# Kernel optimization log

Hardware: AMD Instinct MI355X
Metric: run time of the kernel (lower is better)

## Reference

```python
import jax, jax.numpy as jnp
import numpy as np

TOP_K = 2
CAPACITY_FACTOR = 1.0


def _ffn(x, w1, w2):
    # SwiGLU FFN: x [N, D], w1 [D, 2F], w2 [F, D]
    h = x @ w1
    x1, x2 = jnp.split(h, 2, axis=-1)
    return (x1 * jax.nn.silu(x2)) @ w2


def setup_inputs() -> dict:
    key = jax.random.key(0)
    ks = jax.random.split(key, 6)
    B, S, D, F, E_r, E_s = 4, 2048, 2048, 1024, 7, 1
    sc_in = 1.0 / np.sqrt(D)
    sc_mid = 1.0 / np.sqrt(F)
    return {
        "x": jax.random.normal(ks[0], (B, S, D), dtype=jnp.float32),
        "gate_w": jax.random.normal(ks[1], (D, E_r), dtype=jnp.float32) * sc_in,
        "expert_bias": jnp.zeros((E_r,), dtype=jnp.float32),
        "shared_w1": jax.random.normal(ks[2], (E_s, D, 2 * F), dtype=jnp.float32) * sc_in,
        "shared_w2": jax.random.normal(ks[3], (E_s, F, D), dtype=jnp.float32) * sc_mid,
        "routed_w1": jax.random.normal(ks[4], (E_r, D, 2 * F), dtype=jnp.float32) * sc_in,
        "routed_w2": jax.random.normal(ks[5], (E_r, F, D), dtype=jnp.float32) * sc_mid,
    }


def reference(x, gate_w, expert_bias, shared_w1, shared_w2, routed_w1, routed_w2):
    B, S, D = x.shape
    E_r = gate_w.shape[1]
    T = B * S
    capacity = max(1, int(CAPACITY_FACTOR * T / E_r))
    flat_x = x.reshape(T, D)

    # shared experts: applied to every token, summed
    shared_sum = jax.vmap(_ffn, in_axes=(None, 0, 0))(flat_x, shared_w1, shared_w2).sum(0)

    # gating (eval mode: no noise, no dropout)
    gate_logits = flat_x @ gate_w + expert_bias  # [T, E_r]
    aff = jax.nn.sigmoid(gate_logits)
    _, topk_idx = jax.lax.top_k(aff, TOP_K)  # [T, K]
    # mask[t, e] = expert e is among token t's top-k
    mask = (topk_idx[:, :, None] == jnp.arange(E_r)[None, None, :]).any(axis=1)  # [T, E_r]

    # per-expert capacity selection: keep top-`capacity` masked tokens by affinity
    score = jnp.where(mask, aff, -1.0).T  # [E_r, T]; aff >= 0 so -1 sorts last
    _, sel_idx = jax.lax.top_k(score, capacity)  # [E_r, capacity] token ids
    kept = jnp.take_along_axis(mask.T, sel_idx, axis=1)  # [E_r, cap]
    w = jnp.where(kept, jnp.take_along_axis(aff.T, sel_idx, axis=1), 0.0)  # [E_r, cap]

    # grouped gather -> FFN -> weighted scatter-add
    inp = flat_x[sel_idx]  # [E_r, cap, D]
    out = jax.vmap(_ffn)(inp, routed_w1, routed_w2)  # [E_r, cap, D]
    routed_sum = jnp.zeros_like(flat_x).at[sel_idx].add(out * w[:, :, None])

    return (shared_sum + routed_sum).reshape(B, S, D)
```

## Files before the change

kernel.cpp:

```cpp
#include <hip/hip_runtime.h>
#include <hip/hip_bf16.h>

typedef unsigned long long u64;
typedef __bf16 bf16x8 __attribute__((ext_vector_type(8)));
typedef float f32x4 __attribute__((ext_vector_type(4)));
typedef unsigned short ushort8_t __attribute__((ext_vector_type(8)));

#define TOKS 8192
#define DMODEL 2048
#define FD 1024
#define NEXP 7
#define CAP 1170
#define CAPP 1280
#define URT 134

#define MFMA16(a, b, c) __builtin_amdgcn_mfma_f32_16x16x32_bf16(a, b, c, 0, 0, 0)

__device__ __forceinline__ unsigned short f2bf(float f) {
  __hip_bfloat16 b = __float2bfloat16(f);
  return __builtin_bit_cast(unsigned short, b);
}
__device__ __forceinline__ float bf2f(unsigned short u) {
  __hip_bfloat16 b = __builtin_bit_cast(__hip_bfloat16, u);
  return __bfloat162float(b);
}
__device__ __forceinline__ void gload_lds16(const void* g, void* l) {
  __builtin_amdgcn_global_load_lds(
      (const __attribute__((address_space(1))) void*)g,
      (__attribute__((address_space(3))) void*)l, 16, 0, 0);
}

__global__ __launch_bounds__(256) void k_conv_gate(
    const float* __restrict__ x, const float* __restrict__ gw,
    const float* __restrict__ bias, unsigned short* __restrict__ xb,
    u64* __restrict__ keys) {
  const int t = blockIdx.x;
  const int tid = threadIdx.x;
  const int lane = tid & 63, wv = tid >> 6;
  const float* xr = x + (long)t * DMODEL;
  const int i0 = tid * 8;
  float4 v0 = *(const float4*)&xr[i0];
  float4 v1 = *(const float4*)&xr[i0 + 4];
  float xv[8] = {v0.x, v0.y, v0.z, v0.w, v1.x, v1.y, v1.z, v1.w};
  ushort8_t o;
#pragma unroll
  for (int j = 0; j < 8; ++j) o[j] = f2bf(xv[j]);
  *(ushort8_t*)&xb[(long)t * DMODEL + i0] = o;
  double acc[NEXP];
#pragma unroll
  for (int e = 0; e < NEXP; ++e) acc[e] = 0.0;
#pragma unroll
  for (int j = 0; j < 8; ++j) {
    const float* g = gw + (long)(i0 + j) * NEXP;
    double xd = (double)xv[j];
#pragma unroll
    for (int e = 0; e < NEXP; ++e) acc[e] += xd * (double)g[e];
  }
#pragma unroll
  for (int e = 0; e < NEXP; ++e)
    for (int off = 32; off > 0; off >>= 1)
      acc[e] += __shfl_down(acc[e], off, 64);
  __shared__ double red[4][NEXP];
  if (lane == 0)
#pragma unroll
    for (int e = 0; e < NEXP; ++e) red[wv][e] = acc[e];
  __syncthreads();
  if (tid == 0) {
    float aff[NEXP];
#pragma unroll
    for (int e = 0; e < NEXP; ++e) {
      double lg = red[0][e] + red[1][e] + red[2][e] + red[3][e] + (double)bias[e];
      aff[e] = (float)(1.0 / (1.0 + exp(-lg)));
    }
    int i1 = 0;
    for (int e = 1; e < NEXP; ++e) if (aff[e] > aff[i1]) i1 = e;
    int i2 = -1;
    for (int e = 0; e < NEXP; ++e) {
      if (e == i1) continue;
      if (i2 < 0 || aff[e] > aff[i2]) i2 = e;
    }
#pragma unroll
    for (int e = 0; e < NEXP; ++e) {
      u64 key = (u64)(0xFFFFFFFFu - (unsigned)t);
      if (e == i1 || e == i2) key |= ((u64)__float_as_uint(aff[e])) << 32;
      keys[(long)e * TOKS + t] = key;
    }
  }
}

template <bool PERM>
__global__ void k_transpose_bf16(const float* __restrict__ in0,
                                 const float* __restrict__ inr,
                                 unsigned short* __restrict__ out,
                                 int R, int C) {
  __shared__ float tile[32][33];
  int z = blockIdx.z;
  const float* in = (z == 0) ? in0 : (inr + (long)(z - 1) * R * C);
  unsigned short* o = out + (long)z * R * C;
  int c0 = blockIdx.x * 32;
  int r0 = blockIdx.y * 32;
  int tx = threadIdx.x, ty = threadIdx.y;
#pragma unroll
  for (int k = 0; k < 4; ++k)
    tile[ty + 8 * k][tx] = in[(long)(r0 + ty + 8 * k) * C + c0 + tx];
  __syncthreads();
#pragma unroll
  for (int k = 0; k < 4; ++k) {
    int c = c0 + ty + 8 * k;
    long orow = PERM ? (long)(((c & 1023) >> 4) * 32 + ((c >> 10) << 4) + (c & 15))
                     : (long)c;
    o[orow * R + r0 + tx] = f2bf(tile[tx][ty + 8 * k]);
  }
}

__global__ __launch_bounds__(1024) void k_select(
    const u64* __restrict__ keys, int* __restrict__ sel,
    float* __restrict__ selw, unsigned* __restrict__ cnt,
    int* __restrict__ inv) {
  __shared__ unsigned hist[256];
  __shared__ u64 s_prefix;
  __shared__ unsigned s_k;
  __shared__ unsigned s_cnt;
  const int e = blockIdx.x;
  const u64* kk = keys + (long)e * TOKS;
  const int tid = threadIdx.x;
  if (tid == 0) { s_prefix = 0; s_k = CAP; s_cnt = 0; }
  __syncthreads();
  for (int shift = 56; shift >= 0; shift -= 8) {
    if (tid < 256) hist[tid] = 0;
    __syncthreads();
    u64 pref = s_prefix;
    for (int i = tid; i < TOKS; i += 1024) {
      u64 key = kk[i];
      bool match = (shift == 56) || ((key >> (shift + 8)) == pref);
      if (match) atomicAdd(&hist[(unsigned)(key >> shift) & 255u], 1u);
    }
    __syncthreads();
    if (tid == 0) {
      unsigned k = s_k, cum = 0;
      for (int b = 255; b >= 0; --b) {
        unsigned c = hist[b];
        if (cum + c >= k) {
          s_prefix = (s_prefix << 8) | (unsigned)b;
          s_k = k - cum;
          break;
        }
        cum += c;
      }
    }
    __syncthreads();
  }
  const u64 T = s_prefix;
  for (int i = tid; i < TOKS; i += 1024) {
    u64 key = kk[i];
    if (key >= T) {
      unsigned p = atomicAdd(&s_cnt, 1u);
      int tok = (int)(0xFFFFFFFFu - (unsigned)(key & 0xFFFFFFFFull));
      unsigned vb = (unsigned)(key >> 32);
      sel[e * CAPP + p] = tok;
      selw[e * CAPP + p] = vb ? __uint_as_float(vb) : 0.0f;
      if (vb) {
        unsigned pos = atomicAdd(&cnt[tok], 1u);
        inv[tok * 2 + pos] = e * CAPP + (int)p;
      }
    }
  }
  for (int i = CAP + tid; i < CAPP; i += 1024) {
    sel[e * CAPP + i] = 0;
    selw[e * CAPP + i] = 0.0f;
  }
}

__global__ __launch_bounds__(256) void k_combine(
    float* __restrict__ out, const unsigned short* __restrict__ rout,
    const int* __restrict__ inv, const unsigned* __restrict__ cnt) {
  const int tok = blockIdx.x;
  const unsigned c = cnt[tok];
  if (c == 0) return;
  int i0 = inv[tok * 2];
  int i1 = (c > 1) ? inv[tok * 2 + 1] : -1;
  if (c > 1 && i1 < i0) { int t = i0; i0 = i1; i1 = t; }
  const int col = threadIdx.x * 8;
  float* o = out + (long)tok * DMODEL + col;
  float4 v0 = *(float4*)o;
  float4 v1 = *(float4*)(o + 4);
  ushort8_t r0 = *(const ushort8_t*)&rout[(long)i0 * DMODEL + col];
  v0.x += bf2f(r0[0]); v0.y += bf2f(r0[1]); v0.z += bf2f(r0[2]); v0.w += bf2f(r0[3]);
  v1.x += bf2f(r0[4]); v1.y += bf2f(r0[5]); v1.z += bf2f(r0[6]); v1.w += bf2f(r0[7]);
  if (c > 1) {
    ushort8_t r1 = *(const ushort8_t*)&rout[(long)i1 * DMODEL + col];
    v0.x += bf2f(r1[0]); v0.y += bf2f(r1[1]); v0.z += bf2f(r1[2]); v0.w += bf2f(r1[3]);
    v1.x += bf2f(r1[4]); v1.y += bf2f(r1[5]); v1.z += bf2f(r1[6]); v1.w += bf2f(r1[7]);
  }
  *(float4*)o = v0;
  *(float4*)(o + 4) = v1;
}

template <int WHICH>
__global__ __launch_bounds__(256, 4) void k_ffn(
    const unsigned short* __restrict__ Abase,
    const unsigned short* __restrict__ Wbase,
    unsigned short* __restrict__ a_all, float* __restrict__ out,
    unsigned short* __restrict__ r_out,
    const int* __restrict__ sel, const float* __restrict__ selw) {
  constexpr int K = (WHICH == 1) ? DMODEL : FD;
  constexpr int N = (WHICH == 1) ? 2 * FD : DMODEL;
  constexpr int nk = K >> 5;
  __shared__ unsigned short lds[2][8192];
  const int tid = threadIdx.x;
  const int w = tid >> 6;
  const int lane = tid & 63;

  int lin = blockIdx.x + ((int)blockIdx.y << 4);
  int gt = (lin & 7) * 268 + (lin >> 3);
  int ct, rt;
  int su;
  if (gt < 2048) { su = gt >> 7; int rr = gt & 127; ct = rr >> 3; rt = rr & 7; }
  else           { su = 16;      int rr = gt - 2048; ct = rr / 6; rt = rr % 6; }
  const int by_u = su * 8 + rt;
  const int bx = ct;

  int e, zw, m0l;
  if (by_u < 64) { e = -1; zw = 0; m0l = by_u << 7; }
  else { int q = by_u - 64; e = q / 10; zw = e + 1; m0l = (q % 10) << 7; }
  const long crow0_u = (e < 0) ? (long)m0l : (8192 + (long)e * CAPP + m0l);
  const long n0 = (long)bx * 128;
  const unsigned short* Bm = Wbase + (long)zw * N * K;

  const int r_ = (w << 4) + (lane >> 2);
  const int p_ = lane & 3;
  const unsigned short* aSrc[2];
  const unsigned short* bSrc[2];
#pragma unroll
  for (int c = 0; c < 2; ++c) {
    int rsg = c * 64 + r_;
    int q = p_ ^ ((rsg >> 1) & 3);
    long arow;
    if (WHICH == 1)
      arow = (e < 0) ? (long)(m0l + rsg) : (long)sel[e * CAPP + m0l + rsg];
    else
      arow = crow0_u + rsg;
    aSrc[c] = Abase + arow * (long)K + q * 8;
    bSrc[c] = Bm + (n0 + rsg) * (long)K + q * 8;
  }
  const int dst0 = tid * 8;

  auto STAGE = [&](int buf, int kt) {
    const long ko = (long)kt * 32;
#pragma unroll
    for (int c = 0; c < 2; ++c) {
      gload_lds16(aSrc[c] + ko, &lds[buf][c * 2048 + dst0]);
      gload_lds16(bSrc[c] + ko, &lds[buf][4096 + c * 2048 + dst0]);
    }
  };

  const int wr = w >> 1, wc = w & 1;
  const int lr = lane & 15, kq = lane >> 4;
  const int slot = (kq ^ ((lr >> 1) & 3)) * 8;
  const int aRow = wr * 64 + lr;
  const int bRow = wc * 64 + lr;

  STAGE(0, 0);
  asm volatile("s_waitcnt vmcnt(0)" ::: "memory");
  __builtin_amdgcn_sched_barrier(0);
  __builtin_amdgcn_s_barrier();
  __builtin_amdgcn_sched_barrier(0);

  f32x4 acc[4][4] = {};
  int cur = 0;

#pragma unroll 1
  for (int kt = 0; kt < nk; ++kt) {
    if (kt + 1 < nk) STAGE(cur ^ 1, kt + 1);
    const unsigned short* aSeg = &lds[cur][0];
    const unsigned short* bSeg = &lds[cur][4096];
    bf16x8 af[4], bf[4];
#pragma unroll
    for (int m = 0; m < 4; ++m)
      af[m] = *(const bf16x8*)&aSeg[(aRow + m * 16) * 32 + slot];
#pragma unroll
    for (int n = 0; n < 4; ++n)
      bf[n] = *(const bf16x8*)&bSeg[(bRow + n * 16) * 32 + slot];
    asm volatile("s_waitcnt lgkmcnt(0)" ::: "memory");
    __builtin_amdgcn_sched_barrier(0);
    __builtin_amdgcn_s_setprio(1);
#pragma unroll
    for (int m = 0; m < 4; ++m)
#pragma unroll
      for (int n = 0; n < 4; ++n)
        acc[m][n] = MFMA16(af[m], bf[n], acc[m][n]);
    __builtin_amdgcn_s_setprio(0);
    asm volatile("s_waitcnt vmcnt(0)" ::: "memory");
    __builtin_amdgcn_sched_barrier(0);
    __builtin_amdgcn_s_barrier();
    __builtin_amdgcn_sched_barrier(0);
    cur ^= 1;
  }

  const int r0q = (lane >> 4) * 4;
  const int cc = lane & 15;

  if (WHICH == 1) {
    const long gcol0 = (n0 >> 1) + wc * 32;
#pragma unroll
    for (int m = 0; m < 4; ++m)
#pragma unroll
      for (int rj = 0; rj < 4; ++rj) {
        long row = crow0_u + wr * 64 + m * 16 + r0q + rj;
#pragma unroll
        for (int q2 = 0; q2 < 2; ++q2) {
          float x1v = acc[m][2 * q2][rj];
          float x2v = acc[m][2 * q2 + 1][rj];
          float s = x2v / (1.0f + __expf(-x2v));
          a_all[row * FD + gcol0 + q2 * 16 + cc] = f2bf(x1v * s);
        }
      }
  } else {
    const long ccol0 = n0 + wc * 64;
    if (e < 0) {
#pragma unroll
      for (int m = 0; m < 4; ++m)
#pragma unroll
        for (int rj = 0; rj < 4; ++rj) {
          long row = m0l + wr * 64 + m * 16 + r0q + rj;
#pragma unroll
          for (int n = 0; n < 4; ++n)
            out[row * DMODEL + ccol0 + n * 16 + cc] = acc[m][n][rj];
        }
    } else {
#pragma unroll
      for (int m = 0; m < 4; ++m)
#pragma unroll
        for (int rj = 0; rj < 4; ++rj) {
          int lrow = m0l + wr * 64 + m * 16 + r0q + rj;
          float wgt = selw[e * CAPP + lrow];
          unsigned short* C = r_out + ((long)e * CAPP + lrow) * DMODEL;
#pragma unroll
          for (int n = 0; n < 4; ++n)
            C[ccol0 + n * 16 + cc] = f2bf(acc[m][n][rj] * wgt);
        }
    }
  }
}

extern "C" void kernel_launch(void* const* d_in, const int* in_sizes, int n_in,
                              void* d_out, int out_size, void* d_ws,
                              size_t ws_size, hipStream_t stream) {
  (void)in_sizes; (void)n_in; (void)out_size; (void)ws_size;
  const float* x = (const float*)d_in[0];
  const float* gw = (const float*)d_in[1];
  const float* eb = (const float*)d_in[2];
  const float* sw1 = (const float*)d_in[3];
  const float* sw2 = (const float*)d_in[4];
  const float* rw1 = (const float*)d_in[5];
  const float* rw2 = (const float*)d_in[6];
  float* out = (float*)d_out;

  char* ws = (char*)d_ws;
  size_t off = 0;
  auto alloc = [&](size_t bytes) {
    size_t o = off;
    off += (bytes + 255) & ~(size_t)255;
    return o;
  };
  unsigned short* xb    = (unsigned short*)(ws + alloc((size_t)TOKS * DMODEL * 2));
  unsigned short* w1t   = (unsigned short*)(ws + alloc((size_t)8 * DMODEL * (2 * FD) * 2));
  unsigned short* w2t   = (unsigned short*)(ws + alloc((size_t)8 * DMODEL * FD * 2));
  unsigned short* a_all = (unsigned short*)(ws + alloc((size_t)(TOKS + NEXP * CAPP) * FD * 2));
  unsigned short* r_out = (unsigned short*)(ws + alloc((size_t)NEXP * CAPP * DMODEL * 2));
  u64* keys = (u64*)(ws + alloc((size_t)NEXP * TOKS * 8));
  int* sel  = (int*)(ws + alloc((size_t)NEXP * CAPP * 4));
  float* selw = (float*)(ws + alloc((size_t)NEXP * CAPP * 4));
  unsigned* cnt = (unsigned*)(ws + alloc((size_t)TOKS * 4));
  int* inv = (int*)(ws + alloc((size_t)TOKS * 2 * 4));

  k_conv_gate<<<TOKS, 256, 0, stream>>>(x, gw, eb, xb, keys);
  dim3 tb(32, 8);
  k_transpose_bf16<true><<<dim3(64, 64, 8), tb, 0, stream>>>(sw1, rw1, w1t, DMODEL, 2 * FD);
  k_transpose_bf16<false><<<dim3(64, 32, 8), tb, 0, stream>>>(sw2, rw2, w2t, FD, DMODEL);
  hipMemsetAsync(cnt, 0, (size_t)TOKS * 4, stream);
  k_select<<<NEXP, 1024, 0, stream>>>(keys, sel, selw, cnt, inv);
  k_ffn<1><<<dim3(16, URT), 256, 0, stream>>>(xb, w1t, a_all, nullptr, nullptr,
                                              sel, nullptr);
  k_ffn<2><<<dim3(16, URT), 256, 0, stream>>>(a_all, w2t, nullptr, out, r_out,
                                              nullptr, selw);
  k_combine<<<TOKS, 256, 0, stream>>>(out, r_out, inv, cnt);
}
```

Before: 495.8 us.

## Enlarge FFN GEMM tiles to 256x128 with 512 threads and vectorize weight transpose

The FFN GEMM kernels move from 128x128 tiles with 256 threads to 256x128 tiles with 512 threads (8 waves), so each B tile is reused across twice as many rows. The block-to-tile mapping is rewritten so that each XCD gets a column pair. The weight transpose kernel switches to 64x64 tiles with float4 loads and 8-wide bf16 stores. The point is to cut global traffic for weights and speed up the conversion, at the cost of more LDS per block, which may lower occupancy. The unseen epilogue has to match the new row layout and the wave indexing (wr = w>>1 now spans 4 row groups), and that is not visible here.

```diff
diff --git a/kernel.cpp b/kernel.cpp
--- a/kernel.cpp
+++ b/kernel.cpp
@@ -12,7 +12,7 @@
 #define NEXP 7
 #define CAP 1170
 #define CAPP 1280
-#define URT 134
+#define URT256 67
 
 #define MFMA16(a, b, c) __builtin_amdgcn_mfma_f32_16x16x32_bf16(a, b, c, 0, 0, 0)
 
@@ -89,27 +89,39 @@
 }
 
 template <bool PERM>
-__global__ void k_transpose_bf16(const float* __restrict__ in0,
-                                 const float* __restrict__ inr,
-                                 unsigned short* __restrict__ out,
-                                 int R, int C) {
-  __shared__ float tile[32][33];
+__global__ __launch_bounds__(256) void k_transpose64(
+    const float* __restrict__ in0, const float* __restrict__ inr,
+    unsigned short* __restrict__ out, int R, int C) {
+  __shared__ unsigned short t[64][68];
   int z = blockIdx.z;
   const float* in = (z == 0) ? in0 : (inr + (long)(z - 1) * R * C);
   unsigned short* o = out + (long)z * R * C;
-  int c0 = blockIdx.x * 32;
-  int r0 = blockIdx.y * 32;
-  int tx = threadIdx.x, ty = threadIdx.y;
-#pragma unroll
-  for (int k = 0; k < 4; ++k)
-    tile[ty + 8 * k][tx] = in[(long)(r0 + ty + 8 * k) * C + c0 + tx];
+  const int c0 = blockIdx.x * 64;
+  const int r0 = blockIdx.y * 64;
+  const int tid = threadIdx.x;
+  const int lrow = tid >> 4;
+  const int lc4 = (tid & 15) * 4;
+#pragma unroll
+  for (int i = 0; i < 4; ++i) {
+    int r = lrow + i * 16;
+    float4 v = *(const float4*)&in[(long)(r0 + r) * C + c0 + lc4];
+    t[r][lc4 + 0] = f2bf(v.x);
+    t[r][lc4 + 1] = f2bf(v.y);
+    t[r][lc4 + 2] = f2bf(v.z);
+    t[r][lc4 + 3] = f2bf(v.w);
+  }
   __syncthreads();
-#pragma unroll
-  for (int k = 0; k < 4; ++k) {
-    int c = c0 + ty + 8 * k;
-    long orow = PERM ? (long)(((c & 1023) >> 4) * 32 + ((c >> 10) << 4) + (c & 15))
-                     : (long)c;
-    o[orow * R + r0 + tx] = f2bf(tile[tx][ty + 8 * k]);
+  const int lc = tid >> 2;
+  const int c = c0 + lc;
+  const long orow = PERM ? (long)(((c & 1023) >> 4) * 32 + ((c >> 10) << 4) + (c & 15))
+                         : (long)c;
+#pragma unroll
+  for (int j = 0; j < 2; ++j) {
+    int rloc = ((tid & 3) + j * 4) * 8;
+    ushort8_t o8;
+#pragma unroll
+    for (int q = 0; q < 8; ++q) o8[q] = t[rloc + q][lc];
+    *(ushort8_t*)&o[orow * R + r0 + rloc] = o8;
   }
 }
 
@@ -197,7 +209,7 @@
 }
 
 template <int WHICH>
-__global__ __launch_bounds__(256, 4) void k_ffn(
+__global__ __launch_bounds__(512, 4) void k_ffn(
     const unsigned short* __restrict__ Abase,
     const unsigned short* __restrict__ Wbase,
     unsigned short* __restrict__ a_all, float* __restrict__ out,
@@ -206,52 +218,52 @@
   constexpr int K = (WHICH == 1) ? DMODEL : FD;
   constexpr int N = (WHICH == 1) ? 2 * FD : DMODEL;
   constexpr int nk = K >> 5;
-  __shared__ unsigned short lds[2][8192];
+  constexpr int ASH = 256 * 32;
+  __shared__ unsigned short lds[2][ASH + 128 * 32];
   const int tid = threadIdx.x;
   const int w = tid >> 6;
   const int lane = tid & 63;
 
   int lin = blockIdx.x + ((int)blockIdx.y << 4);
-  int gt = (lin & 7) * 268 + (lin >> 3);
-  int ct, rt;
-  int su;
-  if (gt < 2048) { su = gt >> 7; int rr = gt & 127; ct = rr >> 3; rt = rr & 7; }
-  else           { su = 16;      int rr = gt - 2048; ct = rr / 6; rt = rr % 6; }
-  const int by_u = su * 8 + rt;
-  const int bx = ct;
+  int xcd = lin & 7;
+  int tt = lin >> 3;
+  int colh = (tt >= URT256) ? 1 : 0;
+  int by_u = tt - colh * URT256;
+  int bx = xcd * 2 + colh;
 
   int e, zw, m0l;
-  if (by_u < 64) { e = -1; zw = 0; m0l = by_u << 7; }
-  else { int q = by_u - 64; e = q / 10; zw = e + 1; m0l = (q % 10) << 7; }
+  if (by_u < 32) { e = -1; zw = 0; m0l = by_u << 8; }
+  else { int q = by_u - 32; e = q / 5; zw = e + 1; m0l = (q % 5) << 8; }
   const long crow0_u = (e < 0) ? (long)m0l : (8192 + (long)e * CAPP + m0l);
   const long n0 = (long)bx * 128;
   const unsigned short* Bm = Wbase + (long)zw * N * K;
 
-  const int r_ = (w << 4) + (lane >> 2);
-  const int p_ = lane & 3;
   const unsigned short* aSrc[2];
-  const unsigned short* bSrc[2];
-#pragma unroll
-  for (int c = 0; c < 2; ++c) {
-    int rsg = c * 64 + r_;
-    int q = p_ ^ ((rsg >> 1) & 3);
+  const unsigned short* bSrc;
+#pragma unroll
+  for (int j = 0; j < 2; ++j) {
+    int r = w * 32 + j * 16 + (lane >> 2);
+    int q = (lane & 3) ^ ((r >> 1) & 3);
     long arow;
     if (WHICH == 1)
-      arow = (e < 0) ? (long)(m0l + rsg) : (long)sel[e * CAPP + m0l + rsg];
+      arow = (e < 0) ? (long)(m0l + r) : (long)sel[e * CAPP + m0l + r];
     else
-      arow = crow0_u + rsg;
-    aSrc[c] = Abase + arow * (long)K + q * 8;
-    bSrc[c] = Bm + (n0 + rsg) * (long)K + q * 8;
-  }
-  const int dst0 = tid * 8;
+      arow = crow0_u + r;
+    aSrc[j] = Abase + arow * (long)K + q * 8;
+  }
+  {
+    int r = w * 16 + (lane >> 2);
+    int q = (lane & 3) ^ ((r >> 1) & 3);
+    bSrc = Bm + (n0 + r) * (long)K + q * 8;
+  }
+  const int dstA0 = (w * 128 + lane) * 8;
+  const int dstB0 = ASH + (w * 64 + lane) * 8;
 
   auto STAGE = [&](int buf, int kt) {
     const long ko = (long)kt * 32;
-#pragma unroll
-    for (int c = 0; c < 2; ++c) {
-      gload_lds16(aSrc[c] + ko, &lds[buf][c * 2048 + dst0]);
-      gload_lds16(bSrc[c] + ko, &lds[buf][4096 + c * 2048 + dst0]);
-    }
+    gload_lds16(aSrc[0] + ko, &lds[buf][dstA0]);
+    gload_lds16(aSrc[1] + ko, &lds[buf][dstA0 + 512]);
+    gload_lds16(bSrc + ko, &lds[buf][dstB0]);
   };
 
   const int wr = w >> 1, wc = w & 1;
@@ -273,7 +285,7 @@
   for (int kt = 0; kt < nk; ++kt) {
     if (kt + 1 < nk) STAGE(cur ^ 1, kt + 1);
     const unsigned short* aSeg = &lds[cur][0];
-    const unsigned short* bSeg = &lds[cur][4096];
+    const unsigned short* bSeg = &lds[cur][ASH];
     bf16x8 af[4], bf[4];
 #pragma unroll
     for (int m = 0; m < 4; ++m)
@@ -375,14 +387,13 @@
   int* inv = (int*)(ws + alloc((size_t)TOKS * 2 * 4));
 
   k_conv_gate<<<TOKS, 256, 0, stream>>>(x, gw, eb, xb, keys);
-  dim3 tb(32, 8);
-  k_transpose_bf16<true><<<dim3(64, 64, 8), tb, 0, stream>>>(sw1, rw1, w1t, DMODEL, 2 * FD);
-  k_transpose_bf16<false><<<dim3(64, 32, 8), tb, 0, stream>>>(sw2, rw2, w2t, FD, DMODEL);
+  k_transpose64<true><<<dim3(32, 32, 8), 256, 0, stream>>>(sw1, rw1, w1t, DMODEL, 2 * FD);
+  k_transpose64<false><<<dim3(32, 16, 8), 256, 0, stream>>>(sw2, rw2, w2t, FD, DMODEL);
   hipMemsetAsync(cnt, 0, (size_t)TOKS * 4, stream);
   k_select<<<NEXP, 1024, 0, stream>>>(keys, sel, selw, cnt, inv);
-  k_ffn<1><<<dim3(16, URT), 256, 0, stream>>>(xb, w1t, a_all, nullptr, nullptr,
-                                              sel, nullptr);
-  k_ffn<2><<<dim3(16, URT), 256, 0, stream>>>(a_all, w2t, nullptr, out, r_out,
-                                              nullptr, selw);
+  k_ffn<1><<<dim3(16, URT256), 512, 0, stream>>>(xb, w1t, a_all, nullptr, nullptr,
+                                                 sel, nullptr);
+  k_ffn<2><<<dim3(16, URT256), 512, 0, stream>>>(a_all, w2t, nullptr, out, r_out,
+                                                 nullptr, selw);
   k_combine<<<TOKS, 256, 0, stream>>>(out, r_out, inv, cnt);
 }
```

New measurement: 521.0 us. 5.1% more time.

## Replace 128x128 FFN GEMM with 256x256 tile, 8-wave, interleaved LDS pipeline

Applied to the files above, without the earlier changes.

The two grouped FFN GEMM kernels move from 128x128 output tiles with 4 waves to 256x256 tiles with 8 waves (512 threads), a K-step of 64 and 128 KB of dynamic LDS. Loads are split into four segments (two A halves, two B halves) and issued between MFMA phases, so global-to-LDS transfers overlap compute within each iteration. The LDS layout uses an XOR swizzle. The larger tile raises arithmetic intensity and cuts redundant global traffic. In exchange the grid is much smaller, the old L2-friendly block remapping is dropped, and occupancy per CU is lower, which may hurt load balance and latency hiding. The 128 KB dynamic LDS launch also does not appear to raise any max-dynamic-shared-memory attribute.

```diff
diff --git a/kernel.cpp b/kernel.cpp
--- a/kernel.cpp
+++ b/kernel.cpp
@@ -12,7 +12,7 @@
 #define NEXP 7
 #define CAP 1170
 #define CAPP 1280
-#define URT 134
+#define URT256 67
 
 #define MFMA16(a, b, c) __builtin_amdgcn_mfma_f32_16x16x32_bf16(a, b, c, 0, 0, 0)
 
@@ -197,105 +197,175 @@
 }
 
 template <int WHICH>
-__global__ __launch_bounds__(256, 4) void k_ffn(
+__global__ __launch_bounds__(512, 2) void k_ffn8(
     const unsigned short* __restrict__ Abase,
     const unsigned short* __restrict__ Wbase,
     unsigned short* __restrict__ a_all, float* __restrict__ out,
     unsigned short* __restrict__ r_out,
     const int* __restrict__ sel, const float* __restrict__ selw) {
   constexpr int K = (WHICH == 1) ? DMODEL : FD;
-  constexpr int N = (WHICH == 1) ? 2 * FD : DMODEL;
-  constexpr int nk = K >> 5;
-  __shared__ unsigned short lds[2][8192];
+  constexpr int N = 2048;
+  constexpr int nk = K >> 6;
+  extern __shared__ unsigned short lds[];
   const int tid = threadIdx.x;
   const int w = tid >> 6;
   const int lane = tid & 63;
 
-  int lin = blockIdx.x + ((int)blockIdx.y << 4);
-  int gt = (lin & 7) * 268 + (lin >> 3);
-  int ct, rt;
-  int su;
-  if (gt < 2048) { su = gt >> 7; int rr = gt & 127; ct = rr >> 3; rt = rr & 7; }
-  else           { su = 16;      int rr = gt - 2048; ct = rr / 6; rt = rr % 6; }
-  const int by_u = su * 8 + rt;
-  const int bx = ct;
+  const int bx = blockIdx.x;
+  const int by_u = blockIdx.y;
 
   int e, zw, m0l;
-  if (by_u < 64) { e = -1; zw = 0; m0l = by_u << 7; }
-  else { int q = by_u - 64; e = q / 10; zw = e + 1; m0l = (q % 10) << 7; }
+  if (by_u < 32) { e = -1; zw = 0; m0l = by_u << 8; }
+  else { int q = by_u - 32; e = q / 5; zw = e + 1; m0l = (q % 5) << 8; }
   const long crow0_u = (e < 0) ? (long)m0l : (8192 + (long)e * CAPP + m0l);
-  const long n0 = (long)bx * 128;
+  const long n0 = (long)bx * 256;
   const unsigned short* Bm = Wbase + (long)zw * N * K;
 
-  const int r_ = (w << 4) + (lane >> 2);
-  const int p_ = lane & 3;
-  const unsigned short* aSrc[2];
-  const unsigned short* bSrc[2];
-#pragma unroll
-  for (int c = 0; c < 2; ++c) {
-    int rsg = c * 64 + r_;
-    int q = p_ ^ ((rsg >> 1) & 3);
-    long arow;
-    if (WHICH == 1)
-      arow = (e < 0) ? (long)(m0l + rsg) : (long)sel[e * CAPP + m0l + rsg];
-    else
-      arow = crow0_u + rsg;
-    aSrc[c] = Abase + arow * (long)K + q * 8;
-    bSrc[c] = Bm + (n0 + rsg) * (long)K + q * 8;
-  }
-  const int dst0 = tid * 8;
-
-  auto STAGE = [&](int buf, int kt) {
-    const long ko = (long)kt * 32;
-#pragma unroll
-    for (int c = 0; c < 2; ++c) {
-      gload_lds16(aSrc[c] + ko, &lds[buf][c * 2048 + dst0]);
-      gload_lds16(bSrc[c] + ko, &lds[buf][4096 + c * 2048 + dst0]);
-    }
+  const int wr = w >> 2;
+  const int wc = w & 3;
+  const int lr = lane & 15;
+  const int kq = lane >> 4;
+
+  const unsigned short* aP[2][2];
+  const unsigned short* bP[2][2];
+  int dstOff[2];
+#pragma unroll
+  for (int j = 0; j < 2; ++j) {
+    int L = w * 128 + j * 64 + lane;
+    int r = L >> 3;
+    int cEl = ((L & 7) * 8) ^ ((r & 7) * 8);
+    dstOff[j] = (w * 2 + j) * 512;
+#pragma unroll
+    for (int h = 0; h < 2; ++h) {
+      long ar;
+      if (WHICH == 1)
+        ar = (e < 0) ? (long)(m0l + h * 128 + r)
+                     : (long)sel[e * CAPP + m0l + h * 128 + r];
+      else
+        ar = crow0_u + h * 128 + r;
+      aP[h][j] = Abase + ar * (long)K + cEl;
+      bP[h][j] = Bm + (n0 + h * 128 + r) * (long)K + cEl;
+    }
+  }
+
+  auto STAGE = [&](int seg, int d, int ts) {
+    unsigned short* base = lds + ((d << 2) + seg) * 8192;
+    const unsigned short *p0, *p1;
+    if (seg < 2) { p0 = aP[seg][0]; p1 = aP[seg][1]; }
+    else         { p0 = bP[seg - 2][0]; p1 = bP[seg - 2][1]; }
+    long ko = (long)ts * 64;
+    gload_lds16(p0 + ko, base + dstOff[0]);
+    gload_lds16(p1 + ko, base + dstOff[1]);
   };
 
-  const int wr = w >> 1, wc = w & 1;
-  const int lr = lane & 15, kq = lane >> 4;
-  const int slot = (kq ^ ((lr >> 1) & 3)) * 8;
-  const int aRow = wr * 64 + lr;
-  const int bRow = wc * 64 + lr;
-
-  STAGE(0, 0);
-  asm volatile("s_waitcnt vmcnt(0)" ::: "memory");
+  const int aSegT = wr;
+  const int bSegT = 2 + (wc >> 1);
+  const int colSw0 = (kq * 8) ^ ((lr & 7) * 8);
+  const int colSw1 = (32 + kq * 8) ^ ((lr & 7) * 8);
+  const int bRow = (wc & 1) * 64 + lr;
+
+  STAGE(0, 0, 0); STAGE(1, 0, 0); STAGE(2, 0, 0); STAGE(3, 0, 0);
+  if (nk > 1) { STAGE(0, 1, 1); STAGE(1, 1, 1); }
+  else        { STAGE(0, 1, 0); STAGE(1, 1, 0); }
+  asm volatile("s_waitcnt vmcnt(4)" ::: "memory");
   __builtin_amdgcn_sched_barrier(0);
   __builtin_amdgcn_s_barrier();
   __builtin_amdgcn_sched_barrier(0);
 
-  f32x4 acc[4][4] = {};
-  int cur = 0;
+  f32x4 acc[8][4] = {};
 
 #pragma unroll 1
-  for (int kt = 0; kt < nk; ++kt) {
-    if (kt + 1 < nk) STAGE(cur ^ 1, kt + 1);
-    const unsigned short* aSeg = &lds[cur][0];
-    const unsigned short* bSeg = &lds[cur][4096];
-    bf16x8 af[4], bf[4];
-#pragma unroll
-    for (int m = 0; m < 4; ++m)
-      af[m] = *(const bf16x8*)&aSeg[(aRow + m * 16) * 32 + slot];
-#pragma unroll
-    for (int n = 0; n < 4; ++n)
-      bf[n] = *(const bf16x8*)&bSeg[(bRow + n * 16) * 32 + slot];
+  for (int T = 0; T < nk; ++T) {
+    const int d = T & 1, dn = d ^ 1;
+    int t1 = T + 1; if (t1 >= nk) t1 -= nk;
+    int t2 = T + 2; if (t2 >= nk) t2 -= nk;
+    const unsigned short* aSeg = lds + ((d << 2) + aSegT) * 8192;
+    const unsigned short* bSeg = lds + ((d << 2) + bSegT) * 8192;
+    bf16x8 af[8], b0, b1;
+
+#pragma unroll
+    for (int m = 0; m < 8; ++m)
+      af[m] = *(const bf16x8*)&aSeg[(m * 16 + lr) * 64 + colSw0];
+    b0 = *(const bf16x8*)&bSeg[(bRow + 0) * 64 + colSw0];
+    b1 = *(const bf16x8*)&bSeg[(bRow + 16) * 64 + colSw0];
+    __builtin_amdgcn_sched_barrier(0);
+    STAGE(2, dn, t1);
+    __builtin_amdgcn_sched_barrier(0);
+    __builtin_amdgcn_s_barrier();
     asm volatile("s_waitcnt lgkmcnt(0)" ::: "memory");
     __builtin_amdgcn_sched_barrier(0);
     __builtin_amdgcn_s_setprio(1);
 #pragma unroll
-    for (int m = 0; m < 4; ++m)
-#pragma unroll
-      for (int n = 0; n < 4; ++n)
-        acc[m][n] = MFMA16(af[m], bf[n], acc[m][n]);
+    for (int m = 0; m < 8; ++m) {
+      acc[m][0] = MFMA16(af[m], b0, acc[m][0]);
+      acc[m][1] = MFMA16(af[m], b1, acc[m][1]);
+    }
     __builtin_amdgcn_s_setprio(0);
-    asm volatile("s_waitcnt vmcnt(0)" ::: "memory");
-    __builtin_amdgcn_sched_barrier(0);
-    __builtin_amdgcn_s_barrier();
-    __builtin_amdgcn_sched_barrier(0);
-    cur ^= 1;
-  }
+    __builtin_amdgcn_sched_barrier(0);
+    __builtin_amdgcn_s_barrier();
+    __builtin_amdgcn_sched_barrier(0);
+
+    b0 = *(const bf16x8*)&bSeg[(bRow + 32) * 64 + colSw0];
+    b1 = *(const bf16x8*)&bSeg[(bRow + 48) * 64 + colSw0];
+    __builtin_amdgcn_sched_barrier(0);
+    STAGE(3, dn, t1);
+    __builtin_amdgcn_sched_barrier(0);
+    __builtin_amdgcn_s_barrier();
+    asm volatile("s_waitcnt lgkmcnt(0)" ::: "memory");
+    __builtin_amdgcn_sched_barrier(0);
+    __builtin_amdgcn_s_setprio(1);
+#pragma unroll
+    for (int m = 0; m < 8; ++m) {
+      acc[m][2] = MFMA16(af[m], b0, acc[m][2]);
+      acc[m][3] = MFMA16(af[m], b1, acc[m][3]);
+    }
+    __builtin_amdgcn_s_setprio(0);
+    __builtin_amdgcn_sched_barrier(0);
+    __builtin_amdgcn_s_barrier();
+    __builtin_amdgcn_sched_barrier(0);
+
+#pragma unroll
+    for (int m = 0; m < 8; ++m)
+      af[m] = *(const bf16x8*)&aSeg[(m * 16 + lr) * 64 + colSw1];
+    b0 = *(const bf16x8*)&bSeg[(bRow + 0) * 64 + colSw1];
+    b1 = *(const bf16x8*)&bSeg[(bRow + 16) * 64 + colSw1];
+    __builtin_amdgcn_sched_barrier(0);
+    __builtin_amdgcn_s_barrier();
+    asm volatile("s_waitcnt lgkmcnt(0)" ::: "memory");
+    __builtin_amdgcn_sched_barrier(0);
+    __builtin_amdgcn_s_setprio(1);
+#pragma unroll
+    for (int m = 0; m < 8; ++m) {
+      acc[m][0] = MFMA16(af[m], b0, acc[m][0]);
+      acc[m][1] = MFMA16(af[m], b1, acc[m][1]);
+    }
+    __builtin_amdgcn_s_setprio(0);
+    __builtin_amdgcn_sched_barrier(0);
+    __builtin_amdgcn_s_barrier();
+    __builtin_amdgcn_sched_barrier(0);
+
+    b0 = *(const bf16x8*)&bSeg[(bRow + 32) * 64 + colSw1];
+    b1 = *(const bf16x8*)&bSeg[(bRow + 48) * 64 + colSw1];
+    __builtin_amdgcn_sched_barrier(0);
+    STAGE(0, d, t2);
+    STAGE(1, d, t2);
+    asm volatile("s_waitcnt vmcnt(4)" ::: "memory");
+    __builtin_amdgcn_sched_barrier(0);
+    __builtin_amdgcn_s_barrier();
+    asm volatile("s_waitcnt lgkmcnt(0)" ::: "memory");
+    __builtin_amdgcn_sched_barrier(0);
+    __builtin_amdgcn_s_setprio(1);
+#pragma unroll
+    for (int m = 0; m < 8; ++m) {
+      acc[m][2] = MFMA16(af[m], b0, acc[m][2]);
+      acc[m][3] = MFMA16(af[m], b1, acc[m][3]);
+    }
+    __builtin_amdgcn_s_setprio(0);
+    __builtin_amdgcn_sched_barrier(0);
+    __builtin_amdgcn_s_barrier();
+    __builtin_amdgcn_sched_barrier(0);
+  }
+  asm volatile("s_waitcnt vmcnt(0)" ::: "memory");
 
   const int r0q = (lane >> 4) * 4;
   const int cc = lane & 15;
@@ -303,10 +373,10 @@
   if (WHICH == 1) {
     const long gcol0 = (n0 >> 1) + wc * 32;
 #pragma unroll
-    for (int m = 0; m < 4; ++m)
+    for (int m = 0; m < 8; ++m)
 #pragma unroll
       for (int rj = 0; rj < 4; ++rj) {
-        long row = crow0_u + wr * 64 + m * 16 + r0q + rj;
+        long row = crow0_u + wr * 128 + m * 16 + r0q + rj;
 #pragma unroll
         for (int q2 = 0; q2 < 2; ++q2) {
           float x1v = acc[m][2 * q2][rj];
@@ -319,20 +389,20 @@
     const long ccol0 = n0 + wc * 64;
     if (e < 0) {
 #pragma unroll
-      for (int m = 0; m < 4; ++m)
+      for (int m = 0; m < 8; ++m)
 #pragma unroll
         for (int rj = 0; rj < 4; ++rj) {
-          long row = m0l + wr * 64 + m * 16 + r0q + rj;
+          long row = m0l + wr * 128 + m * 16 + r0q + rj;
 #pragma unroll
           for (int n = 0; n < 4; ++n)
             out[row * DMODEL + ccol0 + n * 16 + cc] = acc[m][n][rj];
         }
     } else {
 #pragma unroll
-      for (int m = 0; m < 4; ++m)
+      for (int m = 0; m < 8; ++m)
 #pragma unroll
         for (int rj = 0; rj < 4; ++rj) {
-          int lrow = m0l + wr * 64 + m * 16 + r0q + rj;
+          int lrow = m0l + wr * 128 + m * 16 + r0q + rj;
           float wgt = selw[e * CAPP + lrow];
           unsigned short* C = r_out + ((long)e * CAPP + lrow) * DMODEL;
 #pragma unroll
@@ -374,15 +444,17 @@
   unsigned* cnt = (unsigned*)(ws + alloc((size_t)TOKS * 4));
   int* inv = (int*)(ws + alloc((size_t)TOKS * 2 * 4));
 
+  const size_t LDSB = 131072;
+
   k_conv_gate<<<TOKS, 256, 0, stream>>>(x, gw, eb, xb, keys);
   dim3 tb(32, 8);
   k_transpose_bf16<true><<<dim3(64, 64, 8), tb, 0, stream>>>(sw1, rw1, w1t, DMODEL, 2 * FD);
   k_transpose_bf16<false><<<dim3(64, 32, 8), tb, 0, stream>>>(sw2, rw2, w2t, FD, DMODEL);
   hipMemsetAsync(cnt, 0, (size_t)TOKS * 4, stream);
   k_select<<<NEXP, 1024, 0, stream>>>(keys, sel, selw, cnt, inv);
-  k_ffn<1><<<dim3(16, URT), 256, 0, stream>>>(xb, w1t, a_all, nullptr, nullptr,
-                                              sel, nullptr);
-  k_ffn<2><<<dim3(16, URT), 256, 0, stream>>>(a_all, w2t, nullptr, out, r_out,
-                                              nullptr, selw);
+  k_ffn8<1><<<dim3(8, URT256), 512, LDSB, stream>>>(xb, w1t, a_all, nullptr,
+                                                    nullptr, sel, nullptr);
+  k_ffn8<2><<<dim3(8, URT256), 512, LDSB, stream>>>(a_all, w2t, nullptr, out,
+                                                    r_out, nullptr, selw);
   k_combine<<<TOKS, 256, 0, stream>>>(out, r_out, inv, cnt);
 }
```

Result: no change. 504.3 us (+1.7%).
